# Kernel optimization log

Measured on AMD Instinct MI355X. Metric: run time of the kernel, lower is better.

## Reference

```python
import jax, jax.numpy as jnp
import numpy as np

B, LQ, LK = 4, 2048, 2048
DQ, DK, DO = 1024, 1024, 1024


def setup_inputs() -> dict:
    key = jax.random.key(0)
    ks = jax.random.split(key, 9)
    s = 0.02
    return {
        "query_input": jax.random.normal(ks[0], (B, LQ, DQ), jnp.float32),
        "key_input": jax.random.normal(ks[1], (B, LK, DK), jnp.float32),
        "value_input": jax.random.normal(ks[2], (B, LK, DK), jnp.float32),
        "Wq": jax.random.normal(ks[3], (DQ, DO), jnp.float32) * s,
        "bq": jax.random.normal(ks[4], (DO,), jnp.float32) * s,
        "Wk": jax.random.normal(ks[5], (DK, DO), jnp.float32) * s,
        "bk": jax.random.normal(ks[6], (DO,), jnp.float32) * s,
        "Wv": jax.random.normal(ks[7], (DK, DO), jnp.float32) * s,
        "bv": jax.random.normal(ks[8], (DO,), jnp.float32) * s,
    }


def reference(query_input, key_input, value_input, Wq, bq, Wk, bk, Wv, bv):
    scale = jnp.asarray(DO, query_input.dtype) ** 0.5
    q = query_input @ Wq + bq              # [B, Lq, D]
    k = key_input @ Wk + bk                # [B, Lk, D]
    v = value_input @ Wv + bv              # [B, Lk, D]
    attn = jnp.einsum("bqd,bkd->bqk", q, k) / scale
    attn = jax.nn.softmax(attn, axis=-1)
    return jnp.einsum("bqk,bkd->bqd", attn, v)
```

## Files before the change

kernel.cpp:

```cpp
#include <hip/hip_runtime.h>

typedef _Float16 f16x8 __attribute__((ext_vector_type(8)));
typedef _Float16 f16x4 __attribute__((ext_vector_type(4)));
typedef float f32x4 __attribute__((ext_vector_type(4)));

__device__ __forceinline__ void lds_load16(const _Float16* g, _Float16* l) {
    __builtin_amdgcn_global_load_lds(
        (const __attribute__((address_space(1))) void*)g,
        (__attribute__((address_space(3))) void*)l,
        16, 0, 0);
}

template <int MODE>
__global__ __launch_bounds__(256, 4)
void gemm_core(const _Float16* A0, const _Float16* B0, void* C0, const float* b0,
               const _Float16* A1, const _Float16* B1, void* C1, const float* b1,
               const _Float16* A2, const _Float16* B2, void* C2, const float* b2,
               float* rowsum)
{
    constexpr int BN = (MODE == 5) ? 64 : 128;
    constexpr int NJ = BN / 32;
    const int z = blockIdx.z;
    const int bx = blockIdx.x, by = blockIdx.y;

    __shared__ __align__(16) _Float16 As[2][128 * 32];
    __shared__ __align__(16) _Float16 Bs[2][BN * 32];

    const int t    = threadIdx.x;
    const int w    = t >> 6;
    const int lane = t & 63;
    const int ln   = lane & 15;
    const int kq   = lane >> 4;
    const int wm   = (w & 1) * 64;
    const int wn   = (w >> 1) * (BN / 2);

    const _Float16* A;
    const _Float16* B;
    size_t cbase = 0;
    int lda, ldb, K, m0, n0;

    if (MODE == 0) {
        const int tmy = bx * 8 + (by >> 3);
        const int tnx = by & 7;
        A = z == 0 ? A0 : z == 1 ? A1 : A2;
        B = z == 0 ? B0 : z == 1 ? B1 : B2;
        lda = 1024; ldb = 1024; K = 1024;
        m0 = (z == 2 ? tnx : tmy) * 128;
        n0 = (z == 2 ? tmy : tnx) * 128;
    } else if (MODE == 3) {
        const int tm = (bx & 7) * 2 + (by >> 3);
        const int tn = (bx >> 3) * 8 + (by & 7);
        A = A0 + (size_t)z * 2048 * 1024;
        B = B0 + (size_t)z * 2048 * 1024;
        cbase = (size_t)z * 2048 * 2048;
        rowsum += z * 2048;
        lda = 1024; ldb = 1024; K = 1024;
        m0 = tm * 128; n0 = tn * 128;
    } else {
        const int tm = (bx & 7) * 2 + (by >> 3);
        const int tn = (bx >> 3) * 8 + (by & 7);
        A = A0 + (size_t)z * 2048 * 2048;
        B = B0 + (size_t)z * 2048;
        cbase = (size_t)z * 2048 * 1024;
        rowsum += z * 2048;
        lda = 2048; ldb = 8192; K = 2048;
        m0 = tm * 128; n0 = tn * BN;
    }

    const _Float16* gA0 = A + (size_t)(m0 + (t >> 2)) * lda + (t & 3) * 8;
    const _Float16* gA1 = gA0 + (size_t)64 * lda;
    const _Float16* gB0 = B + (size_t)(n0 + (t >> 2)) * ldb + (t & 3) * 8;
    const _Float16* gB1 = (BN == 128) ? gB0 + (size_t)64 * ldb : nullptr;

    auto stage = [&](int b, int k0) {
        lds_load16(gA0 + k0, As[b] + w * 512);
        lds_load16(gA1 + k0, As[b] + 2048 + w * 512);
        lds_load16(gB0 + k0, Bs[b] + w * 512);
        if (BN == 128) lds_load16(gB1 + k0, Bs[b] + 2048 + w * 512);
    };

    f32x4 acc[4][NJ] = {};

    stage(0, 0);
    int cur = 0;
#pragma unroll 2
    for (int k0 = 0; k0 < K; k0 += 32) {
        __syncthreads();
        if (k0 + 32 < K) stage(cur ^ 1, k0 + 32);
        const _Float16* Ab = As[cur];
        const _Float16* Bb = Bs[cur];
        f16x8 af[4], bf[NJ];
#pragma unroll
        for (int i = 0; i < 4; ++i)
            af[i] = *(const f16x8*)(Ab + (wm + i * 16 + ln) * 32 + kq * 8);
#pragma unroll
        for (int j = 0; j < NJ; ++j)
            bf[j] = *(const f16x8*)(Bb + (wn + j * 16 + ln) * 32 + kq * 8);
#pragma unroll
        for (int i = 0; i < 4; ++i)
#pragma unroll
            for (int j = 0; j < NJ; ++j)
                acc[i][j] = __builtin_amdgcn_mfma_f32_16x16x32_f16(af[i], bf[j], acc[i][j], 0, 0, 0);
        cur ^= 1;
    }

    if (MODE == 0) {
        _Float16* Cp = (_Float16*)(z == 0 ? C0 : z == 1 ? C1 : C2);
        const float* bp = z == 0 ? b0 : z == 1 ? b1 : b2;
        const int ldc = (z == 2) ? 8192 : 1024;
#pragma unroll
        for (int i = 0; i < 4; ++i) {
            const int rbase = m0 + wm + i * 16 + kq * 4;
#pragma unroll
            for (int j = 0; j < 4; ++j) {
                const int gcol = n0 + wn + j * 16 + ln;
#pragma unroll
                for (int r = 0; r < 4; ++r) {
                    float vv = acc[i][j][r] + (z == 2 ? bp[rbase + r] : bp[gcol]);
                    Cp[(size_t)(rbase + r) * ldc + gcol] = (_Float16)vv;
                }
            }
        }
    } else if (MODE == 3) {
        _Float16* Ch = (_Float16*)C0;
#pragma unroll
        for (int i = 0; i < 4; ++i) {
            const int rbase = m0 + wm + i * 16 + kq * 4;
            float rs[4] = {0.f, 0.f, 0.f, 0.f};
#pragma unroll
            for (int j = 0; j < 4; ++j) {
                const int gcol = n0 + wn + j * 16 + ln;
#pragma unroll
                for (int r = 0; r < 4; ++r) {
                    float e = __expf(acc[i][j][r] * 0.03125f);
                    Ch[cbase + (size_t)(rbase + r) * 2048 + gcol] = (_Float16)e;
                    rs[r] += e;
                }
            }
#pragma unroll
            for (int r = 0; r < 4; ++r) {
                float s = rs[r];
                s += __shfl_xor(s, 1);
                s += __shfl_xor(s, 2);
                s += __shfl_xor(s, 4);
                s += __shfl_xor(s, 8);
                if (ln == 0) atomicAdd(&rowsum[rbase + r], s);
            }
        }
    } else {
        float* Cf = (float*)C0;
#pragma unroll
        for (int i = 0; i < 4; ++i) {
            const int rbase = m0 + wm + i * 16 + kq * 4;
            float inv[4];
#pragma unroll
            for (int r = 0; r < 4; ++r) inv[r] = 1.f / rowsum[rbase + r];
#pragma unroll
            for (int j = 0; j < NJ; ++j) {
                const int gcol = n0 + wn + j * 16 + ln;
#pragma unroll
                for (int r = 0; r < 4; ++r)
                    Cf[cbase + (size_t)(rbase + r) * 1024 + gcol] = acc[i][j][r] * inv[r];
            }
        }
    }
}

__global__ __launch_bounds__(256)
void prep(const float4* __restrict__ x0, _Float16* __restrict__ y0,
          const float4* __restrict__ x1, _Float16* __restrict__ y1,
          const float4* __restrict__ x2, _Float16* __restrict__ y2,
          const float* __restrict__ W0, _Float16* __restrict__ T0,
          const float* __restrict__ W1, _Float16* __restrict__ T1,
          const float* __restrict__ W2, _Float16* __restrict__ T2,
          float* __restrict__ rowsum)
{
    if (blockIdx.y < 3) {
        const size_t i = (size_t)blockIdx.x * 256 + threadIdx.x;
        const float4* x = blockIdx.y == 0 ? x0 : blockIdx.y == 1 ? x1 : x2;
        _Float16*    yy = blockIdx.y == 0 ? y0 : blockIdx.y == 1 ? y1 : y2;
        float4 f = x[i];
        f16x4 o = { (_Float16)f.x, (_Float16)f.y, (_Float16)f.z, (_Float16)f.w };
        *(f16x4*)(yy + i * 4) = o;
        if (blockIdx.y == 0 && blockIdx.x < 32)
            rowsum[blockIdx.x * 256 + threadIdx.x] = 0.f;
        return;
    }
    if (blockIdx.x >= 3072) return;
    const int zz = blockIdx.x >> 10;
    const int tb = blockIdx.x & 1023;
    const float* W = zz == 0 ? W0 : zz == 1 ? W1 : W2;
    _Float16*   WT = zz == 0 ? T0 : zz == 1 ? T1 : T2;
    __shared__ float tile[32][33];
    const int bxs = (tb & 31) * 32;
    const int bys = (tb >> 5) * 32;
    const int tx = threadIdx.x & 31;
    const int ty = threadIdx.x >> 5;
#pragma unroll
    for (int i = ty; i < 32; i += 8)
        tile[i][tx] = W[(size_t)(bys + i) * 1024 + bxs + tx];
    __syncthreads();
#pragma unroll
    for (int i = ty; i < 32; i += 8)
        WT[(size_t)(bxs + i) * 1024 + bys + tx] = (_Float16)tile[tx][i];
}

extern "C" void kernel_launch(void* const* d_in, const int* in_sizes, int n_in,
                              void* d_out, int out_size, void* d_ws, size_t ws_size,
                              hipStream_t stream)
{
    const float* Xq = (const float*)d_in[0];
    const float* Xk = (const float*)d_in[1];
    const float* Xv = (const float*)d_in[2];
    const float* Wq = (const float*)d_in[3];
    const float* bq = (const float*)d_in[4];
    const float* Wk = (const float*)d_in[5];
    const float* bk = (const float*)d_in[6];
    const float* Wv = (const float*)d_in[7];
    const float* bv = (const float*)d_in[8];
    float* out = (float*)d_out;

    const size_t XN = (size_t)8192 * 1024;
    const size_t WN = (size_t)1024 * 1024;

    _Float16* ws  = (_Float16*)d_ws;
    _Float16* Xqh = ws;
    _Float16* Xkh = Xqh + XN;
    _Float16* Xvh = Xkh + XN;
    _Float16* WqT = Xvh + XN;
    _Float16* WkT = WqT + WN;
    _Float16* WvT = WkT + WN;
    _Float16* qh  = WvT + WN;
    _Float16* kh  = qh + XN;
    _Float16* vT  = kh + XN;
    _Float16* S   = vT + XN;
    float* rowsum = (float*)(S + (size_t)4 * 2048 * 2048);

    {
        dim3 g(8192, 4);
        prep<<<g, 256, 0, stream>>>((const float4*)Xq, Xqh,
                                    (const float4*)Xk, Xkh,
                                    (const float4*)Xv, Xvh,
                                    Wq, WqT, Wk, WkT, Wv, WvT, rowsum);
    }

    {
        dim3 g(8, 64, 3);
        gemm_core<0><<<g, 256, 0, stream>>>(
            Xqh, WqT, qh, bq,
            Xkh, WkT, kh, bk,
            WvT, Xvh, vT, bv,
            nullptr);
    }

    {
        dim3 g(16, 16, 4);
        gemm_core<3><<<g, 256, 0, stream>>>(
            qh, kh, S, nullptr,
            nullptr, nullptr, nullptr, nullptr,
            nullptr, nullptr, nullptr, nullptr,
            rowsum);
    }

    {
        dim3 g(16, 16, 4);
        gemm_core<5><<<g, 256, 0, stream>>>(
            S, vT, out, nullptr,
            nullptr, nullptr, nullptr, nullptr,
            nullptr, nullptr, nullptr, nullptr,
            rowsum);
    }
}
```

Baseline: 327.6 us.

## Enlarge GEMM tiles to 256x128 with XOR-swizzled LDS layout

```diff
diff --git a/kernel.cpp b/kernel.cpp
--- a/kernel.cpp
+++ b/kernel.cpp
@@ -12,74 +12,74 @@
 }
 
 template <int MODE>
-__global__ __launch_bounds__(256, 4)
+__global__ __launch_bounds__(256, 2)
 void gemm_core(const _Float16* A0, const _Float16* B0, void* C0, const float* b0,
                const _Float16* A1, const _Float16* B1, void* C1, const float* b1,
                const _Float16* A2, const _Float16* B2, void* C2, const float* b2,
                float* rowsum)
 {
-    constexpr int BN = (MODE == 5) ? 64 : 128;
-    constexpr int NJ = BN / 32;
+    constexpr int K   = (MODE == 5) ? 2048 : 1024;
+    constexpr int LDA = (MODE == 5) ? 2048 : 1024;
+    constexpr int LDB = (MODE == 5) ? 8192 : 1024;
+
     const int z = blockIdx.z;
     const int bx = blockIdx.x, by = blockIdx.y;
 
-    __shared__ __align__(16) _Float16 As[2][128 * 32];
-    __shared__ __align__(16) _Float16 Bs[2][BN * 32];
+    __shared__ __align__(16) _Float16 As[2][256 * 32];
+    __shared__ __align__(16) _Float16 Bs[2][128 * 32];
 
     const int t    = threadIdx.x;
     const int w    = t >> 6;
     const int lane = t & 63;
     const int ln   = lane & 15;
     const int kq   = lane >> 4;
-    const int wm   = (w & 1) * 64;
-    const int wn   = (w >> 1) * (BN / 2);
+    const int wm   = (w & 1) * 128;
+    const int wn   = (w >> 1) * 64;
 
     const _Float16* A;
     const _Float16* B;
     size_t cbase = 0;
-    int lda, ldb, K, m0, n0;
+    int m0, n0;
 
     if (MODE == 0) {
-        const int tmy = bx * 8 + (by >> 3);
-        const int tnx = by & 7;
         A = z == 0 ? A0 : z == 1 ? A1 : A2;
         B = z == 0 ? B0 : z == 1 ? B1 : B2;
-        lda = 1024; ldb = 1024; K = 1024;
-        m0 = (z == 2 ? tnx : tmy) * 128;
-        n0 = (z == 2 ? tmy : tnx) * 128;
+        if (z == 2) { m0 = (by & 3) * 256; n0 = ((by >> 2) * 8 + bx) * 128; }
+        else        { m0 = by * 256;       n0 = bx * 128; }
     } else if (MODE == 3) {
-        const int tm = (bx & 7) * 2 + (by >> 3);
-        const int tn = (bx >> 3) * 8 + (by & 7);
         A = A0 + (size_t)z * 2048 * 1024;
         B = B0 + (size_t)z * 2048 * 1024;
         cbase = (size_t)z * 2048 * 2048;
         rowsum += z * 2048;
-        lda = 1024; ldb = 1024; K = 1024;
-        m0 = tm * 128; n0 = tn * 128;
+        m0 = (by >> 1) * 256;
+        n0 = ((by & 1) * 8 + bx) * 128;
     } else {
-        const int tm = (bx & 7) * 2 + (by >> 3);
-        const int tn = (bx >> 3) * 8 + (by & 7);
         A = A0 + (size_t)z * 2048 * 2048;
         B = B0 + (size_t)z * 2048;
         cbase = (size_t)z * 2048 * 1024;
         rowsum += z * 2048;
-        lda = 2048; ldb = 8192; K = 2048;
-        m0 = tm * 128; n0 = tn * BN;
-    }
-
-    const _Float16* gA0 = A + (size_t)(m0 + (t >> 2)) * lda + (t & 3) * 8;
-    const _Float16* gA1 = gA0 + (size_t)64 * lda;
-    const _Float16* gB0 = B + (size_t)(n0 + (t >> 2)) * ldb + (t & 3) * 8;
-    const _Float16* gB1 = (BN == 128) ? gB0 + (size_t)64 * ldb : nullptr;
+        m0 = by * 256;
+        n0 = bx * 128;
+    }
+
+    const int r4 = t >> 2;
+    const int sc = ((t & 3) ^ ((t >> 3) & 3)) * 8;
+    const _Float16* gA = A + (size_t)(m0 + r4) * LDA + sc;
+    const _Float16* gB = B + (size_t)(n0 + r4) * LDB + sc;
 
     auto stage = [&](int b, int k0) {
-        lds_load16(gA0 + k0, As[b] + w * 512);
-        lds_load16(gA1 + k0, As[b] + 2048 + w * 512);
-        lds_load16(gB0 + k0, Bs[b] + w * 512);
-        if (BN == 128) lds_load16(gB1 + k0, Bs[b] + 2048 + w * 512);
+#pragma unroll
+        for (int s = 0; s < 4; ++s)
+            lds_load16(gA + k0 + (size_t)s * 64 * LDA, As[b] + s * 2048 + w * 512);
+        lds_load16(gB + k0,                     Bs[b] + w * 512);
+        lds_load16(gB + k0 + (size_t)64 * LDB,  Bs[b] + 2048 + w * 512);
     };
 
-    f32x4 acc[4][NJ] = {};
+    const int swz   = (kq ^ ((ln >> 1) & 3)) * 8;
+    const int abase = (wm + ln) * 32 + swz;
+    const int bbase = (wn + ln) * 32 + swz;
+
+    f32x4 acc[8][4] = {};
 
     stage(0, 0);
     int cur = 0;
@@ -87,19 +87,19 @@
     for (int k0 = 0; k0 < K; k0 += 32) {
         __syncthreads();
         if (k0 + 32 < K) stage(cur ^ 1, k0 + 32);
-        const _Float16* Ab = As[cur];
-        const _Float16* Bb = Bs[cur];
-        f16x8 af[4], bf[NJ];
-#pragma unroll
-        for (int i = 0; i < 4; ++i)
-            af[i] = *(const f16x8*)(Ab + (wm + i * 16 + ln) * 32 + kq * 8);
-#pragma unroll
-        for (int j = 0; j < NJ; ++j)
-            bf[j] = *(const f16x8*)(Bb + (wn + j * 16 + ln) * 32 + kq * 8);
-#pragma unroll
-        for (int i = 0; i < 4; ++i)
-#pragma unroll
-            for (int j = 0; j < NJ; ++j)
+        const _Float16* Ab = As[cur] + abase;
+        const _Float16* Bb = Bs[cur] + bbase;
+        f16x8 af[8], bf[4];
+#pragma unroll
+        for (int i = 0; i < 8; ++i)
+            af[i] = *(const f16x8*)(Ab + i * 512);
+#pragma unroll
+        for (int j = 0; j < 4; ++j)
+            bf[j] = *(const f16x8*)(Bb + j * 512);
+#pragma unroll
+        for (int i = 0; i < 8; ++i)
+#pragma unroll
+            for (int j = 0; j < 4; ++j)
                 acc[i][j] = __builtin_amdgcn_mfma_f32_16x16x32_f16(af[i], bf[j], acc[i][j], 0, 0, 0);
         cur ^= 1;
     }
@@ -109,7 +109,7 @@
         const float* bp = z == 0 ? b0 : z == 1 ? b1 : b2;
         const int ldc = (z == 2) ? 8192 : 1024;
 #pragma unroll
-        for (int i = 0; i < 4; ++i) {
+        for (int i = 0; i < 8; ++i) {
             const int rbase = m0 + wm + i * 16 + kq * 4;
 #pragma unroll
             for (int j = 0; j < 4; ++j) {
@@ -124,7 +124,7 @@
     } else if (MODE == 3) {
         _Float16* Ch = (_Float16*)C0;
 #pragma unroll
-        for (int i = 0; i < 4; ++i) {
+        for (int i = 0; i < 8; ++i) {
             const int rbase = m0 + wm + i * 16 + kq * 4;
             float rs[4] = {0.f, 0.f, 0.f, 0.f};
 #pragma unroll
@@ -150,13 +150,13 @@
     } else {
         float* Cf = (float*)C0;
 #pragma unroll
-        for (int i = 0; i < 4; ++i) {
+        for (int i = 0; i < 8; ++i) {
             const int rbase = m0 + wm + i * 16 + kq * 4;
             float inv[4];
 #pragma unroll
             for (int r = 0; r < 4; ++r) inv[r] = 1.f / rowsum[rbase + r];
 #pragma unroll
-            for (int j = 0; j < NJ; ++j) {
+            for (int j = 0; j < 4; ++j) {
                 const int gcol = n0 + wn + j * 16 + ln;
 #pragma unroll
                 for (int r = 0; r < 4; ++r)
@@ -245,7 +245,7 @@
     }
 
     {
-        dim3 g(8, 64, 3);
+        dim3 g(8, 32, 3);
         gemm_core<0><<<g, 256, 0, stream>>>(
             Xqh, WqT, qh, bq,
             Xkh, WkT, kh, bk,
@@ -254,7 +254,7 @@
     }
 
     {
-        dim3 g(16, 16, 4);
+        dim3 g(8, 16, 4);
         gemm_core<3><<<g, 256, 0, stream>>>(
             qh, kh, S, nullptr,
             nullptr, nullptr, nullptr, nullptr,
@@ -263,7 +263,7 @@
     }
 
     {
-        dim3 g(16, 16, 4);
+        dim3 g(8, 8, 4);
         gemm_core<5><<<g, 256, 0, stream>>>(
             S, vT, out, nullptr,
             nullptr, nullptr, nullptr, nullptr,
```

After: 354.4 us. +8.2%, slower.
